# Kernel tuning notes

Hardware: AMD Instinct MI355X
Metric: run time of the kernel (lower is better)

## Reference

```python
import jax, jax.numpy as jnp
import numpy as np

E = 8        # num_experts
TOPK = 2     # num_experts_per_tok
D = 1024     # n_embd
H = 2816     # grok FFN hidden dim (multiple_of-rounded 2/3*4*D)
B, T = 4, 2048
COEFF = 0.01 # moe_aux_loss_coeff


def setup_inputs() -> dict:
    key = jax.random.key(0)
    ks = jax.random.split(key, 8)
    s = 0.02  # weight scale so activations stay well-conditioned
    return {
        "x": jax.random.normal(ks[0], (B, T, D), jnp.float32),
        "gate_w": jax.random.normal(ks[1], (D, E), jnp.float32) * s,
        "expert_gate": jax.random.normal(ks[2], (E, D, H), jnp.float32) * s,
        "expert_up": jax.random.normal(ks[3], (E, D, H), jnp.float32) * s,
        "expert_down": jax.random.normal(ks[4], (E, H, D), jnp.float32) * s,
        "shared_gate": jax.random.normal(ks[5], (D, H), jnp.float32) * s,
        "shared_up": jax.random.normal(ks[6], (D, H), jnp.float32) * s,
        "shared_down": jax.random.normal(ks[7], (H, D), jnp.float32) * s,
    }


def _grok_ffn(x, g, u, d):
    # down(gelu(gate(x)) * up(x)); torch F.gelu default = exact erf gelu
    return (jax.nn.gelu(x @ g, approximate=False) * (x @ u)) @ d


def reference(x, gate_w, expert_gate, expert_up, expert_down,
              shared_gate, shared_up, shared_down):
    Bb, Tt, Dd = x.shape
    N = Bb * Tt
    xf = x.reshape(N, Dd)

    # --- router ---
    logits = (xf @ gate_w).astype(jnp.float32)            # (N, E)
    top_logits, top_idx = jax.lax.top_k(logits, TOPK)     # (N, K)
    top_w = jax.nn.softmax(top_logits, axis=-1)           # (N, K)
    gates = jax.nn.softmax(logits, axis=-1)               # (N, E)
    f = jnp.mean(jax.nn.one_hot(top_idx[:, 0], E, dtype=jnp.float32), axis=0)
    P = gates.mean(axis=0)
    aux_loss = COEFF * E * jnp.sum(f * P)

    # dense combine weights (N, E): 0 for unassigned experts
    comb = jnp.zeros((N, E), xf.dtype).at[
        jnp.arange(N)[:, None], top_idx].add(top_w.astype(xf.dtype))

    # --- experts: loop over small fixed E, weight-masked dense FFN ---
    out = jnp.zeros_like(xf)
    for e in range(E):
        ye = _grok_ffn(xf, expert_gate[e], expert_up[e], expert_down[e])
        out = out + comb[:, e:e + 1] * ye

    out = out.reshape(Bb, Tt, Dd)
    out = out + _grok_ffn(xf, shared_gate, shared_up, shared_down).reshape(Bb, Tt, Dd)
    return out, aux_loss
```

## Files before the change

kernel.cpp:

```cpp
#include <hip/hip_runtime.h>
#include <hip/hip_bf16.h>

#define NTOK 8192
#define DIM  1024
#define HID  2816
#define NI   (2 * HID)
#define ROWS_CAP 26880
#define TC256 104
#define TC128 208

typedef __bf16 bf16x8 __attribute__((ext_vector_type(8)));
typedef float  f32x4  __attribute__((ext_vector_type(4)));

__device__ __forceinline__ unsigned short f2bf(float f) {
  unsigned int x = __float_as_uint(f);
  unsigned int r = (x + 0x7fffu + ((x >> 16) & 1u)) >> 16;
  return (unsigned short)r;
}
__device__ __forceinline__ float gelu_erf(float g) {
  return 0.5f * g * (1.0f + erff(g * 0.70710678118654752f));
}

__device__ __forceinline__ void gload16(const void* g, void* l) {
  __builtin_amdgcn_global_load_lds(
      (__attribute__((address_space(1))) void*)(g),
      (__attribute__((address_space(3))) void*)(l), 16, 0, 0);
}

__device__ __forceinline__ void transpose64(const float* __restrict__ in,
                                            unsigned short* __restrict__ out,
                                            int R, int C, int iloff) {
  __shared__ float t[64][65];
  int c0 = blockIdx.x * 64, r0 = blockIdx.y * 64;
  int tid = threadIdx.x;
  int lr = tid >> 4;
  int lc4 = (tid & 15) * 4;
  #pragma unroll
  for (int it = 0; it < 4; ++it) {
    int row = lr + it * 16;
    float4 v = *(const float4*)(in + (size_t)(r0 + row) * C + c0 + lc4);
    t[row][lc4] = v.x; t[row][lc4 + 1] = v.y;
    t[row][lc4 + 2] = v.z; t[row][lc4 + 3] = v.w;
  }
  __syncthreads();
  #pragma unroll
  for (int it = 0; it < 4; ++it) {
    int cloc = lr + it * 16;
    int c = c0 + cloc;
    int rowil = (iloff < 0) ? c : (((c >> 4) << 5) + (c & 15) + iloff);
    ushort4 w = make_ushort4(f2bf(t[lc4][cloc]), f2bf(t[lc4 + 1][cloc]),
                             f2bf(t[lc4 + 2][cloc]), f2bf(t[lc4 + 3][cloc]));
    *(ushort4*)(out + (size_t)rowil * R + r0 + lc4) = w;
  }
}

__global__ __launch_bounds__(256) void k_transpose_DH(
    const float* __restrict__ eg, const float* __restrict__ eu,
    const float* __restrict__ sg, const float* __restrict__ su,
    unsigned short* __restrict__ WI, unsigned short* __restrict__ SI) {
  int z = blockIdx.z;
  const float* in; unsigned short* out; int off;
  if (z < 8)        { in = eg + (size_t)z * DIM * HID;       out = WI + (size_t)z * NI * DIM; off = 0; }
  else if (z < 16)  { in = eu + (size_t)(z - 8) * DIM * HID; out = WI + (size_t)(z - 8) * NI * DIM; off = 16; }
  else if (z == 16) { in = sg; out = SI; off = 0; }
  else              { in = su; out = SI; off = 16; }
  transpose64(in, out, DIM, HID, off);
}

__global__ __launch_bounds__(256) void k_transpose_HD(
    const float* __restrict__ ed, const float* __restrict__ sd,
    unsigned short* __restrict__ WdT, unsigned short* __restrict__ SdT) {
  int z = blockIdx.z;
  const float* in; unsigned short* out;
  if (z < 8) { in = ed + (size_t)z * HID * DIM; out = WdT + (size_t)z * HID * DIM; }
  else       { in = sd; out = SdT; }
  transpose64(in, out, HID, DIM, -1);
}


__global__ __launch_bounds__(256) void k_router(const float* __restrict__ x,
                                                const float* __restrict__ gw,
                                                unsigned short* __restrict__ xb,
                                                int* __restrict__ top_idx,
                                                float* __restrict__ top_w,
                                                int* __restrict__ counts,
                                                float* __restrict__ f_cnt,
                                                float* __restrict__ P_sum) {
  __shared__ float s_p[8];
  __shared__ int   s_cnt[8];
  __shared__ int   s_f[8];
  int tid = threadIdx.x;
  if (tid < 8) { s_p[tid] = 0.f; s_cnt[tid] = 0; s_f[tid] = 0; }
  __syncthreads();

  int lane = tid & 63, wv = tid >> 6;
  float ploc[8] = {0,0,0,0,0,0,0,0};
  int   cloc[8] = {0,0,0,0,0,0,0,0};
  int   floc[8] = {0,0,0,0,0,0,0,0};

  for (int t = blockIdx.x * 4 + wv; t < NTOK; t += 2048) {
    const float4* xr = (const float4*)(x + (size_t)t * DIM) + lane * 4;
    float4 v0 = xr[0], v1 = xr[1], v2 = xr[2], v3 = xr[3];
    float xv[16] = {v0.x, v0.y, v0.z, v0.w, v1.x, v1.y, v1.z, v1.w,
                    v2.x, v2.y, v2.z, v2.w, v3.x, v3.y, v3.z, v3.w};
    ushort4* xw = (ushort4*)(xb + (size_t)t * DIM + lane * 16);
    #pragma unroll
    for (int q = 0; q < 4; ++q)
      xw[q] = make_ushort4(f2bf(xv[q * 4]), f2bf(xv[q * 4 + 1]),
                           f2bf(xv[q * 4 + 2]), f2bf(xv[q * 4 + 3]));
    float acc[8] = {0.f,0.f,0.f,0.f,0.f,0.f,0.f,0.f};
    #pragma unroll
    for (int i = 0; i < 16; ++i) {
      const float* g = gw + (size_t)(lane * 16 + i) * 8;
      #pragma unroll
      for (int e = 0; e < 8; ++e) acc[e] += xv[i] * g[e];
    }
    #pragma unroll
    for (int e = 0; e < 8; ++e) {
      #pragma unroll
      for (int off = 32; off > 0; off >>= 1)
        acc[e] += __shfl_xor(acc[e], off, 64);
    }
    if (lane == 0) {
      int i1 = 0; float l1 = acc[0];
      #pragma unroll
      for (int e = 1; e < 8; ++e) if (acc[e] > l1) { l1 = acc[e]; i1 = e; }
      int i2 = -1; float l2 = -3.0e38f;
      #pragma unroll
      for (int e = 0; e < 8; ++e) if (e != i1 && acc[e] > l2) { l2 = acc[e]; i2 = e; }
      float e2 = expf(l2 - l1);
      float inv12 = 1.0f / (1.0f + e2);
      top_idx[2 * t] = i1; top_idx[2 * t + 1] = i2;
      top_w[2 * t] = inv12; top_w[2 * t + 1] = e2 * inv12;
      float s = 0.f, p[8];
      #pragma unroll
      for (int e = 0; e < 8; ++e) { p[e] = expf(acc[e] - l1); s += p[e]; }
      float invs = 1.0f / s;
      #pragma unroll
      for (int e = 0; e < 8; ++e) {
        ploc[e] += p[e] * invs;
        cloc[e] += (e == i1) + (e == i2);
        floc[e] += (e == i1);
      }
    }
  }
  if (lane == 0) {
    #pragma unroll
    for (int e = 0; e < 8; ++e) {
      atomicAdd(&s_p[e], ploc[e]);
      atomicAdd(&s_cnt[e], cloc[e]);
      atomicAdd(&s_f[e], floc[e]);
    }
  }
  __syncthreads();
  if (tid < 8) {
    atomicAdd(&P_sum[tid], s_p[tid]);
    atomicAdd(&counts[tid], s_cnt[tid]);
    atomicAdd(&f_cnt[tid], (float)s_f[tid]);
  }
}


__global__ __launch_bounds__(256) void k_setup(const int* __restrict__ counts,
                                               int* __restrict__ cursors,
                                               int* __restrict__ te256,
                                               int* __restrict__ te128,
                                               int* __restrict__ perm,
                                               float* __restrict__ wrow) {
  int t = threadIdx.x;
  for (int r = t; r < ROWS_CAP; r += 256) {
    perm[r] = (r < NTOK) ? r : 0;
    wrow[r] = (r < NTOK) ? 1.0f : 0.0f;
  }
  if (t == 0) {
    int so[8], pe[8];
    int cur = NTOK;
    for (int e = 0; e < 8; ++e) {
      so[e] = cur;
      pe[e] = ((counts[e] + 255) >> 8) << 8;
      cur += pe[e];
    }
    for (int e = 0; e < 8; ++e) cursors[e] = so[e];
    for (int T = 0; T < TC256; ++T) {
      int r0 = T << 8;
      int ex;
      if (T < NTOK / 256) ex = 8;
      else if (r0 < cur) {
        ex = 0;
        for (int e = 0; e < 8; ++e) if (r0 >= so[e] && r0 < so[e] + pe[e]) ex = e;
      } else ex = -1;
      te256[T] = ex;
    }
    for (int ht = 0; ht < TC128; ++ht) {
      int r0 = ht << 7;
      int ex;
      if (ht < NTOK / 128) ex = 8;
      else if (r0 < cur) {
        ex = 0;
        for (int e = 0; e < 8; ++e) if (r0 >= so[e] && r0 < so[e] + pe[e]) ex = e;
      } else ex = -1;
      te128[ht] = ex;
    }
  }
}

__global__ __launch_bounds__(256) void k_scatter(const int* __restrict__ top_idx,
                                                 const float* __restrict__ top_w,
                                                 int* __restrict__ cursors,
                                                 int* __restrict__ perm,
                                                 float* __restrict__ wrow) {
  int i = blockIdx.x * 256 + threadIdx.x;
  if (i < NTOK * 2) {
    int e = top_idx[i];
    float w = top_w[i];
    int slot = atomicAdd(&cursors[e], 1);
    perm[slot] = i >> 1;
    wrow[slot] = w;
  }
}


__global__ __launch_bounds__(512) void k_stageA(const unsigned short* __restrict__ xb,
    const unsigned short* __restrict__ WI, const unsigned short* __restrict__ SI,
    const int* __restrict__ perm, const int* __restrict__ te256,
    unsigned short* __restrict__ h, int T0, int row_base) {
  int T = T0 + blockIdx.y;
  int e = te256[T];
  if (e < 0) return;
  const unsigned short* B = (e < 8) ? WI + (size_t)e * NI * DIM : SI;
  int rows0 = T * 256;
  int c0i = blockIdx.x * 256;

  __shared__ unsigned short As[2][256 * 64];
  __shared__ unsigned short Bs[2][256 * 64];

  int tid = threadIdx.x, lane = tid & 63, w = tid >> 6;
  int wr = w >> 2, wc = w & 3;
  int rlo = lane >> 3;
  int koff = ((lane & 7) ^ rlo) * 8;
  int fr = lane & 15;
  int kby0 = ((lane >> 4) * 16) ^ ((lane & 7) << 4);
  int kby1 = (64 + (lane >> 4) * 16) ^ ((lane & 7) << 4);

  int prow[4];
  #pragma unroll
  for (int i = 0; i < 4; ++i) prow[i] = perm[rows0 + i * 64 + w * 8 + rlo];
  const unsigned short* bsrc[4];
  #pragma unroll
  for (int i = 0; i < 4; ++i)
    bsrc[i] = B + (size_t)(c0i + i * 64 + w * 8 + rlo) * DIM + koff;

  f32x4 acc[8][4] = {};

  #pragma unroll
  for (int i = 0; i < 4; ++i)
    gload16(xb + (size_t)prow[i] * DIM + koff, (char*)As[0] + (i * 64 + w * 8) * 128);
  #pragma unroll
  for (int i = 0; i < 4; ++i)
    gload16(bsrc[i], (char*)Bs[0] + (i * 64 + w * 8) * 128);
  asm volatile("s_waitcnt vmcnt(0)" ::: "memory");
  __builtin_amdgcn_s_barrier();
  __builtin_amdgcn_sched_barrier(0);

  int cur = 0;
  for (int kb = 0; kb < DIM / 64; ++kb) {
    const char* Ab = (const char*)As[cur];
    const char* Bb = (const char*)Bs[cur];
    char* An = (char*)As[cur ^ 1];
    char* Bn = (char*)Bs[cur ^ 1];
    int k1 = (kb + 1) * 64;
    bool pf = (kb < DIM / 64 - 1);
    bf16x8 bfr[4][2];

    #pragma unroll
    for (int q = 0; q < 4; ++q) {
      bf16x8 a[2][2];
      #pragma unroll
      for (int m = 0; m < 2; ++m) {
        const char* ar = Ab + (wr * 128 + (2 * q + m) * 16 + fr) * 128;
        a[m][0] = *(const bf16x8*)(ar + kby0);
        a[m][1] = *(const bf16x8*)(ar + kby1);
      }
      if (q == 0) {
        #pragma unroll
        for (int ni = 0; ni < 4; ++ni) {
          const char* br = Bb + (wc * 64 + ni * 16 + fr) * 128;
          bfr[ni][0] = *(const bf16x8*)(br + kby0);
          bfr[ni][1] = *(const bf16x8*)(br + kby1);
        }
      }
      if (pf) {
        if (q == 0) {
          gload16(xb + (size_t)prow[0] * DIM + k1 + koff, An + (0 * 64 + w * 8) * 128);
          gload16(xb + (size_t)prow[1] * DIM + k1 + koff, An + (1 * 64 + w * 8) * 128);
        } else if (q == 1) {
          gload16(xb + (size_t)prow[2] * DIM + k1 + koff, An + (2 * 64 + w * 8) * 128);
          gload16(xb + (size_t)prow[3] * DIM + k1 + koff, An + (3 * 64 + w * 8) * 128);
        } else if (q == 2) {
          gload16(bsrc[0] + k1, Bn + (0 * 64 + w * 8) * 128);
          gload16(bsrc[1] + k1, Bn + (1 * 64 + w * 8) * 128);
        } else {
          gload16(bsrc[2] + k1, Bn + (2 * 64 + w * 8) * 128);
          gload16(bsrc[3] + k1, Bn + (3 * 64 + w * 8) * 128);
        }
      }
      __builtin_amdgcn_s_barrier();
      __builtin_amdgcn_s_setprio(1);
      #pragma unroll
      for (int kk = 0; kk < 2; ++kk) {
        #pragma unroll
        for (int m = 0; m < 2; ++m) {
          #pragma unroll
          for (int ni = 0; ni < 4; ++ni)
            acc[2 * q + m][ni] = __builtin_amdgcn_mfma_f32_16x16x32_bf16(
                a[m][kk], bfr[ni][kk], acc[2 * q + m][ni], 0, 0, 0);
        }
      }
      __builtin_amdgcn_s_setprio(0);
      if (q < 3) {
        __builtin_amdgcn_s_barrier();
      } else {
        asm volatile("s_waitcnt vmcnt(0)" ::: "memory");
        __builtin_amdgcn_s_barrier();
        __builtin_amdgcn_sched_barrier(0);
      }
    }
    cur ^= 1;
  }

  #pragma unroll
  for (int mi = 0; mi < 8; ++mi) {
    #pragma unroll
    for (int p = 0; p < 2; ++p) {
      #pragma unroll
      for (int j = 0; j < 4; ++j) {
        int rg = rows0 - row_base + wr * 128 + mi * 16 + (lane >> 4) * 4 + j;
        int cg = blockIdx.x * 128 + wc * 32 + p * 16 + fr;
        float g = acc[mi][2 * p][j];
        float u = acc[mi][2 * p + 1][j];
        h[(size_t)rg * HID + cg] = f2bf(gelu_erf(g) * u);
      }
    }
  }
}


template <bool STORE>
__global__ __launch_bounds__(256) void k_stageB(const unsigned short* __restrict__ h,
    const unsigned short* __restrict__ WdT, const unsigned short* __restrict__ SdT,
    const int* __restrict__ perm, const float* __restrict__ wrow,
    const int* __restrict__ te128,
    float* __restrict__ out, int t0, int row_base) {
  int tile = t0 + blockIdx.y;
  int e = te128[tile];
  if (e < 0) return;
  const unsigned short* Bd = (e < 8) ? WdT + (size_t)e * DIM * HID : SdT;
  int rows0 = tile * 128;
  int n0 = blockIdx.x * 128;

  __shared__ unsigned short As[2][128 * 64];
  __shared__ unsigned short Bs[2][128 * 64];

  int tid = threadIdx.x, lane = tid & 63, wv = tid >> 6;
  int wr = wv >> 1, wc = wv & 1;
  int rlo = lane >> 3;
  int koff = (((lane & 7) ^ rlo) * 8);
  int rsw = (lane & 7) << 4;

  f32x4 acc[4][4] = {};

  auto stage = [&](int b, int k0) {
    #pragma unroll
    for (int i = 0; i < 4; ++i) {
      int rb = i * 32 + wv * 8;
      int r = rb + rlo;
      gload16(h + (size_t)(rows0 - row_base + r) * HID + k0 + koff, (char*)As[b] + rb * 128);
      gload16(Bd + (size_t)(n0 + r) * HID + k0 + koff, (char*)Bs[b] + rb * 128);
    }
  };

  auto compute = [&](int b) {
    #pragma unroll
    for (int kk = 0; kk < 2; ++kk) {
      int kbyte = (kk * 64 + (lane >> 4) * 16) ^ rsw;
      bf16x8 a[4], bb[4];
      #pragma unroll
      for (int mi = 0; mi < 4; ++mi)
        a[mi] = *(const bf16x8*)((const char*)As[b] + (wr * 64 + mi * 16 + (lane & 15)) * 128 + kbyte);
      #pragma unroll
      for (int ni = 0; ni < 4; ++ni)
        bb[ni] = *(const bf16x8*)((const char*)Bs[b] + (wc * 64 + ni * 16 + (lane & 15)) * 128 + kbyte);
      #pragma unroll
      for (int mi = 0; mi < 4; ++mi) {
        #pragma unroll
        for (int ni = 0; ni < 4; ++ni)
          acc[mi][ni] = __builtin_amdgcn_mfma_f32_16x16x32_bf16(a[mi], bb[ni], acc[mi][ni], 0, 0, 0);
      }
    }
  };

  stage(0, 0);
  int cur = 0;
  for (int kb = 0; kb < HID / 64 - 1; ++kb) {
    stage(cur ^ 1, (kb + 1) * 64);
    __builtin_amdgcn_sched_barrier(0);
    asm volatile("s_waitcnt vmcnt(8)" ::: "memory");
    __builtin_amdgcn_s_barrier();
    __builtin_amdgcn_sched_barrier(0);
    __builtin_amdgcn_s_setprio(1);
    compute(cur);
    __builtin_amdgcn_s_setprio(0);
    __builtin_amdgcn_s_barrier();
    cur ^= 1;
  }
  asm volatile("s_waitcnt vmcnt(0)" ::: "memory");
  __builtin_amdgcn_s_barrier();
  __builtin_amdgcn_sched_barrier(0);
  compute(cur);

  #pragma unroll
  for (int mi = 0; mi < 4; ++mi) {
    #pragma unroll
    for (int j = 0; j < 4; ++j) {
      int rl = wr * 64 + mi * 16 + (lane >> 4) * 4 + j;
      int token = perm[rows0 + rl];
      float w = wrow[rows0 + rl];
      #pragma unroll
      for (int ni = 0; ni < 4; ++ni) {
        int col = n0 + wc * 64 + ni * 16 + (lane & 15);
        if (STORE) out[(size_t)token * DIM + col] = w * acc[mi][ni][j];
        else atomicAdd(&out[(size_t)token * DIM + col], w * acc[mi][ni][j]);
      }
    }
  }
}


__global__ void k_aux(const float* __restrict__ f_cnt, const float* __restrict__ P_sum,
                      float* __restrict__ aux_out) {
  if (threadIdx.x == 0 && blockIdx.x == 0) {
    float a = 0.f;
    #pragma unroll
    for (int e = 0; e < 8; ++e) a += f_cnt[e] * P_sum[e];
    a *= 0.01f * 8.f / ((float)NTOK * (float)NTOK);
    aux_out[0] = a;
  }
}


extern "C" void kernel_launch(void* const* d_in, const int* in_sizes, int n_in,
                              void* d_out, int out_size, void* d_ws, size_t ws_size,
                              hipStream_t stream) {
  const float* x  = (const float*)d_in[0];
  const float* gw = (const float*)d_in[1];
  const float* eg = (const float*)d_in[2];
  const float* eu = (const float*)d_in[3];
  const float* ed = (const float*)d_in[4];
  const float* sg = (const float*)d_in[5];
  const float* su = (const float*)d_in[6];
  const float* sd = (const float*)d_in[7];
  float* out = (float*)d_out;

  char* ws = (char*)d_ws;
  size_t off = 0;
  auto take = [&](size_t sz) { size_t o = off; off += (sz + 255) & ~(size_t)255; return o; };
  const size_t OFF_XB   = take((size_t)NTOK * DIM * 2);
  const size_t OFF_WI   = take((size_t)8 * NI * DIM * 2);
  const size_t OFF_SI   = take((size_t)NI * DIM * 2);
  const size_t OFF_WDT  = take((size_t)8 * HID * DIM * 2);
  const size_t OFF_SDT  = take((size_t)HID * DIM * 2);
  const size_t OFF_TI   = take((size_t)NTOK * 2 * 4);
  const size_t OFF_TW   = take((size_t)NTOK * 2 * 4);
  const size_t OFF_PERM = take((size_t)ROWS_CAP * 4);
  const size_t OFF_WROW = take((size_t)ROWS_CAP * 4);
  const size_t OFF_STATS= take(256);
  const size_t OFF_CURS = take(256);
  const size_t OFF_TE2  = take(TC256 * 4);
  const size_t OFF_TE1  = take(TC128 * 4);
  const size_t OFF_H    = off;

  const size_t TILE_H_BYTES = (size_t)256 * HID * 2;
  size_t avail = (ws_size > OFF_H) ? (ws_size - OFF_H) : 0;
  int G = (int)((avail / TILE_H_BYTES < (size_t)TC256) ? (avail / TILE_H_BYTES) : (size_t)TC256);
  if (G < 1) return;

  unsigned short* xb  = (unsigned short*)(ws + OFF_XB);
  unsigned short* WI  = (unsigned short*)(ws + OFF_WI);
  unsigned short* SI  = (unsigned short*)(ws + OFF_SI);
  unsigned short* WdT = (unsigned short*)(ws + OFF_WDT);
  unsigned short* SdT = (unsigned short*)(ws + OFF_SDT);
  int* top_idx        = (int*)(ws + OFF_TI);
  float* top_w        = (float*)(ws + OFF_TW);
  int* perm           = (int*)(ws + OFF_PERM);
  float* wrow         = (float*)(ws + OFF_WROW);
  int* counts         = (int*)(ws + OFF_STATS);
  float* f_cnt        = (float*)(ws + OFF_STATS + 32);
  float* P_sum        = (float*)(ws + OFF_STATS + 64);
  int* cursors        = (int*)(ws + OFF_CURS);
  int* te256          = (int*)(ws + OFF_TE2);
  int* te128          = (int*)(ws + OFF_TE1);
  unsigned short* hbuf = (unsigned short*)(ws + OFF_H);

  hipMemsetAsync(ws + OFF_STATS, 0, 256, stream);

  k_transpose_DH<<<dim3(HID / 64, DIM / 64, 18), 256, 0, stream>>>(
      eg, eu, sg, su, WI, SI);
  k_transpose_HD<<<dim3(DIM / 64, HID / 64, 9), 256, 0, stream>>>(
      ed, sd, WdT, SdT);

  k_router<<<512, 256, 0, stream>>>(x, gw, xb, top_idx, top_w, counts, f_cnt, P_sum);
  k_setup<<<1, 256, 0, stream>>>(counts, cursors, te256, te128, perm, wrow);
  k_scatter<<<NTOK * 2 / 256, 256, 0, stream>>>(top_idx, top_w, cursors, perm, wrow);

  for (int T0 = 0; T0 < TC256; T0 += G) {
    int nt = (TC256 - T0 < G) ? (TC256 - T0) : G;
    int row_base = T0 * 256;
    k_stageA<<<dim3(NI / 256, nt), 512, 0, stream>>>(xb, WI, SI, perm, te256,
                                                     hbuf, T0, row_base);
    int h0t = T0 * 2, hn = nt * 2;
    int ns = 0;
    if (h0t < 64) { ns = 64 - h0t; if (ns > hn) ns = hn; }
    int ne = hn - ns;
    if (ns > 0)
      k_stageB<true><<<dim3(DIM / 128, ns), 256, 0, stream>>>(hbuf, WdT, SdT, perm, wrow,
                                                              te128, out, h0t, row_base);
    if (ne > 0)
      k_stageB<false><<<dim3(DIM / 128, ne), 256, 0, stream>>>(hbuf, WdT, SdT, perm, wrow,
                                                               te128, out, h0t + ns, row_base);
  }

  k_aux<<<1, 64, 0, stream>>>(f_cnt, P_sum, out + (size_t)NTOK * DIM);
}
```

Measured before the change: 908.3 us.

## Enlarge down-projection tiles to 256x256 with 8 waves and interleaved prefetch

The down-projection kernel moves from 128x128 tiles with 4 waves to 256x256 tiles with 8 waves, each wave computing a 128x64 sub-tile. Global-to-LDS prefetch of the next K block is split into four chunks interleaved with the MFMA quarters. The separate 128-row tile-to-expert table is removed and the 256-row table is reused. Larger tiles raise arithmetic intensity and cut redundant loads of h and weights, but use 128KB of LDS and more accumulator registers, lowering occupancy. The grid also shrinks to a quarter of the blocks, which may underfill the GPU.

```diff
diff --git a/kernel.cpp b/kernel.cpp
--- a/kernel.cpp
+++ b/kernel.cpp
@@ -7,7 +7,6 @@
 #define NI   (2 * HID)
 #define ROWS_CAP 26880
 #define TC256 104
-#define TC128 208
 
 typedef __bf16 bf16x8 __attribute__((ext_vector_type(8)));
 typedef float  f32x4  __attribute__((ext_vector_type(4)));
@@ -164,7 +163,6 @@
 __global__ __launch_bounds__(256) void k_setup(const int* __restrict__ counts,
                                                int* __restrict__ cursors,
                                                int* __restrict__ te256,
-                                               int* __restrict__ te128,
                                                int* __restrict__ perm,
                                                float* __restrict__ wrow) {
   int t = threadIdx.x;
@@ -190,16 +188,6 @@
         for (int e = 0; e < 8; ++e) if (r0 >= so[e] && r0 < so[e] + pe[e]) ex = e;
       } else ex = -1;
       te256[T] = ex;
-    }
-    for (int ht = 0; ht < TC128; ++ht) {
-      int r0 = ht << 7;
-      int ex;
-      if (ht < NTOK / 128) ex = 8;
-      else if (r0 < cur) {
-        ex = 0;
-        for (int e = 0; e < 8; ++e) if (r0 >= so[e] && r0 < so[e] + pe[e]) ex = e;
-      } else ex = -1;
-      te128[ht] = ex;
     }
   }
 }
@@ -346,90 +334,128 @@
 
 
 template <bool STORE>
-__global__ __launch_bounds__(256) void k_stageB(const unsigned short* __restrict__ h,
+__global__ __launch_bounds__(512) void k_stageB(const unsigned short* __restrict__ h,
     const unsigned short* __restrict__ WdT, const unsigned short* __restrict__ SdT,
     const int* __restrict__ perm, const float* __restrict__ wrow,
-    const int* __restrict__ te128,
-    float* __restrict__ out, int t0, int row_base) {
-  int tile = t0 + blockIdx.y;
-  int e = te128[tile];
+    const int* __restrict__ te256,
+    float* __restrict__ out, int T0, int row_base) {
+  int T = T0 + blockIdx.y;
+  int e = te256[T];
   if (e < 0) return;
   const unsigned short* Bd = (e < 8) ? WdT + (size_t)e * DIM * HID : SdT;
-  int rows0 = tile * 128;
-  int n0 = blockIdx.x * 128;
-
-  __shared__ unsigned short As[2][128 * 64];
-  __shared__ unsigned short Bs[2][128 * 64];
-
-  int tid = threadIdx.x, lane = tid & 63, wv = tid >> 6;
-  int wr = wv >> 1, wc = wv & 1;
+  int rows0 = T * 256;
+  int n0 = blockIdx.x * 256;
+
+  __shared__ unsigned short As[2][256 * 64];
+  __shared__ unsigned short Bs[2][256 * 64];
+
+  int tid = threadIdx.x, lane = tid & 63, w = tid >> 6;
+  int wr = w >> 2, wc = w & 3;
   int rlo = lane >> 3;
-  int koff = (((lane & 7) ^ rlo) * 8);
-  int rsw = (lane & 7) << 4;
-
-  f32x4 acc[4][4] = {};
-
-  auto stage = [&](int b, int k0) {
-    #pragma unroll
-    for (int i = 0; i < 4; ++i) {
-      int rb = i * 32 + wv * 8;
-      int r = rb + rlo;
-      gload16(h + (size_t)(rows0 - row_base + r) * HID + k0 + koff, (char*)As[b] + rb * 128);
-      gload16(Bd + (size_t)(n0 + r) * HID + k0 + koff, (char*)Bs[b] + rb * 128);
-    }
-  };
-
-  auto compute = [&](int b) {
-    #pragma unroll
-    for (int kk = 0; kk < 2; ++kk) {
-      int kbyte = (kk * 64 + (lane >> 4) * 16) ^ rsw;
-      bf16x8 a[4], bb[4];
-      #pragma unroll
-      for (int mi = 0; mi < 4; ++mi)
-        a[mi] = *(const bf16x8*)((const char*)As[b] + (wr * 64 + mi * 16 + (lane & 15)) * 128 + kbyte);
-      #pragma unroll
-      for (int ni = 0; ni < 4; ++ni)
-        bb[ni] = *(const bf16x8*)((const char*)Bs[b] + (wc * 64 + ni * 16 + (lane & 15)) * 128 + kbyte);
-      #pragma unroll
-      for (int mi = 0; mi < 4; ++mi) {
-        #pragma unroll
-        for (int ni = 0; ni < 4; ++ni)
-          acc[mi][ni] = __builtin_amdgcn_mfma_f32_16x16x32_bf16(a[mi], bb[ni], acc[mi][ni], 0, 0, 0);
-      }
-    }
-  };
-
-  stage(0, 0);
-  int cur = 0;
-  for (int kb = 0; kb < HID / 64 - 1; ++kb) {
-    stage(cur ^ 1, (kb + 1) * 64);
-    __builtin_amdgcn_sched_barrier(0);
-    asm volatile("s_waitcnt vmcnt(8)" ::: "memory");
-    __builtin_amdgcn_s_barrier();
-    __builtin_amdgcn_sched_barrier(0);
-    __builtin_amdgcn_s_setprio(1);
-    compute(cur);
-    __builtin_amdgcn_s_setprio(0);
-    __builtin_amdgcn_s_barrier();
-    cur ^= 1;
-  }
+  int koff = ((lane & 7) ^ rlo) * 8;
+  int fr = lane & 15;
+  int kby0 = ((lane >> 4) * 16) ^ ((lane & 7) << 4);
+  int kby1 = (64 + (lane >> 4) * 16) ^ ((lane & 7) << 4);
+
+  const unsigned short* asrc[4];
+  #pragma unroll
+  for (int i = 0; i < 4; ++i)
+    asrc[i] = h + (size_t)(rows0 - row_base + i * 64 + w * 8 + rlo) * HID + koff;
+  const unsigned short* bsrc[4];
+  #pragma unroll
+  for (int i = 0; i < 4; ++i)
+    bsrc[i] = Bd + (size_t)(n0 + i * 64 + w * 8 + rlo) * HID + koff;
+
+  f32x4 acc[8][4] = {};
+
+  #pragma unroll
+  for (int i = 0; i < 4; ++i)
+    gload16(asrc[i], (char*)As[0] + (i * 64 + w * 8) * 128);
+  #pragma unroll
+  for (int i = 0; i < 4; ++i)
+    gload16(bsrc[i], (char*)Bs[0] + (i * 64 + w * 8) * 128);
   asm volatile("s_waitcnt vmcnt(0)" ::: "memory");
   __builtin_amdgcn_s_barrier();
   __builtin_amdgcn_sched_barrier(0);
-  compute(cur);
-
-  #pragma unroll
-  for (int mi = 0; mi < 4; ++mi) {
+
+  int cur = 0;
+  for (int kb = 0; kb < HID / 64; ++kb) {
+    const char* Ab = (const char*)As[cur];
+    const char* Bb = (const char*)Bs[cur];
+    char* An = (char*)As[cur ^ 1];
+    char* Bn = (char*)Bs[cur ^ 1];
+    int k1 = (kb + 1) * 64;
+    bool pf = (kb < HID / 64 - 1);
+    bf16x8 bfr[4][2];
+
+    #pragma unroll
+    for (int q = 0; q < 4; ++q) {
+      bf16x8 a[2][2];
+      #pragma unroll
+      for (int m = 0; m < 2; ++m) {
+        const char* ar = Ab + (wr * 128 + (2 * q + m) * 16 + fr) * 128;
+        a[m][0] = *(const bf16x8*)(ar + kby0);
+        a[m][1] = *(const bf16x8*)(ar + kby1);
+      }
+      if (q == 0) {
+        #pragma unroll
+        for (int ni = 0; ni < 4; ++ni) {
+          const char* br = Bb + (wc * 64 + ni * 16 + fr) * 128;
+          bfr[ni][0] = *(const bf16x8*)(br + kby0);
+          bfr[ni][1] = *(const bf16x8*)(br + kby1);
+        }
+      }
+      if (pf) {
+        if (q == 0) {
+          gload16(asrc[0] + k1, An + (0 * 64 + w * 8) * 128);
+          gload16(asrc[1] + k1, An + (1 * 64 + w * 8) * 128);
+        } else if (q == 1) {
+          gload16(asrc[2] + k1, An + (2 * 64 + w * 8) * 128);
+          gload16(asrc[3] + k1, An + (3 * 64 + w * 8) * 128);
+        } else if (q == 2) {
+          gload16(bsrc[0] + k1, Bn + (0 * 64 + w * 8) * 128);
+          gload16(bsrc[1] + k1, Bn + (1 * 64 + w * 8) * 128);
+        } else {
+          gload16(bsrc[2] + k1, Bn + (2 * 64 + w * 8) * 128);
+          gload16(bsrc[3] + k1, Bn + (3 * 64 + w * 8) * 128);
+        }
+      }
+      __builtin_amdgcn_s_barrier();
+      __builtin_amdgcn_s_setprio(1);
+      #pragma unroll
+      for (int kk = 0; kk < 2; ++kk) {
+        #pragma unroll
+        for (int m = 0; m < 2; ++m) {
+          #pragma unroll
+          for (int ni = 0; ni < 4; ++ni)
+            acc[2 * q + m][ni] = __builtin_amdgcn_mfma_f32_16x16x32_bf16(
+                a[m][kk], bfr[ni][kk], acc[2 * q + m][ni], 0, 0, 0);
+        }
+      }
+      __builtin_amdgcn_s_setprio(0);
+      if (q < 3) {
+        __builtin_amdgcn_s_barrier();
+      } else {
+        asm volatile("s_waitcnt vmcnt(0)" ::: "memory");
+        __builtin_amdgcn_s_barrier();
+        __builtin_amdgcn_sched_barrier(0);
+      }
+    }
+    cur ^= 1;
+  }
+
+  #pragma unroll
+  for (int mi = 0; mi < 8; ++mi) {
     #pragma unroll
     for (int j = 0; j < 4; ++j) {
-      int rl = wr * 64 + mi * 16 + (lane >> 4) * 4 + j;
+      int rl = wr * 128 + mi * 16 + (lane >> 4) * 4 + j;
       int token = perm[rows0 + rl];
-      float w = wrow[rows0 + rl];
+      float wt = wrow[rows0 + rl];
       #pragma unroll
       for (int ni = 0; ni < 4; ++ni) {
-        int col = n0 + wc * 64 + ni * 16 + (lane & 15);
-        if (STORE) out[(size_t)token * DIM + col] = w * acc[mi][ni][j];
-        else atomicAdd(&out[(size_t)token * DIM + col], w * acc[mi][ni][j]);
+        int col = n0 + wc * 64 + ni * 16 + fr;
+        if (STORE) out[(size_t)token * DIM + col] = wt * acc[mi][ni][j];
+        else atomicAdd(&out[(size_t)token * DIM + col], wt * acc[mi][ni][j]);
       }
     }
   }
@@ -476,7 +502,6 @@
   const size_t OFF_STATS= take(256);
   const size_t OFF_CURS = take(256);
   const size_t OFF_TE2  = take(TC256 * 4);
-  const size_t OFF_TE1  = take(TC128 * 4);
   const size_t OFF_H    = off;
 
   const size_t TILE_H_BYTES = (size_t)256 * HID * 2;
@@ -498,7 +523,6 @@
   float* P_sum        = (float*)(ws + OFF_STATS + 64);
   int* cursors        = (int*)(ws + OFF_CURS);
   int* te256          = (int*)(ws + OFF_TE2);
-  int* te128          = (int*)(ws + OFF_TE1);
   unsigned short* hbuf = (unsigned short*)(ws + OFF_H);
 
   hipMemsetAsync(ws + OFF_STATS, 0, 256, stream);
@@ -509,7 +533,7 @@
       ed, sd, WdT, SdT);
 
   k_router<<<512, 256, 0, stream>>>(x, gw, xb, top_idx, top_w, counts, f_cnt, P_sum);
-  k_setup<<<1, 256, 0, stream>>>(counts, cursors, te256, te128, perm, wrow);
+  k_setup<<<1, 256, 0, stream>>>(counts, cursors, te256, perm, wrow);
   k_scatter<<<NTOK * 2 / 256, 256, 0, stream>>>(top_idx, top_w, cursors, perm, wrow);
 
   for (int T0 = 0; T0 < TC256; T0 += G) {
@@ -517,16 +541,15 @@
     int row_base = T0 * 256;
     k_stageA<<<dim3(NI / 256, nt), 512, 0, stream>>>(xb, WI, SI, perm, te256,
                                                      hbuf, T0, row_base);
-    int h0t = T0 * 2, hn = nt * 2;
     int ns = 0;
-    if (h0t < 64) { ns = 64 - h0t; if (ns > hn) ns = hn; }
-    int ne = hn - ns;
+    if (T0 < 32) { ns = 32 - T0; if (ns > nt) ns = nt; }
+    int ne = nt - ns;
     if (ns > 0)
-      k_stageB<true><<<dim3(DIM / 128, ns), 256, 0, stream>>>(hbuf, WdT, SdT, perm, wrow,
-                                                              te128, out, h0t, row_base);
+      k_stageB<true><<<dim3(DIM / 256, ns), 512, 0, stream>>>(hbuf, WdT, SdT, perm, wrow,
+                                                              te256, out, T0, row_base);
     if (ne > 0)
-      k_stageB<false><<<dim3(DIM / 128, ne), 256, 0, stream>>>(hbuf, WdT, SdT, perm, wrow,
-                                                               te128, out, h0t + ns, row_base);
+      k_stageB<false><<<dim3(DIM / 256, ne), 512, 0, stream>>>(hbuf, WdT, SdT, perm, wrow,
+                                                               te256, out, T0 + ns, row_base);
   }
 
   k_aux<<<1, 64, 0, stream>>>(f_cnt, P_sum, out + (size_t)NTOK * DIM);
```

Measured after the change: 961.8 us. +5.9%, slower.
